# Performance work log

Hardware: AMD Instinct MI355X
Metric: run time of the kernel (lower is better)

Reference implementation:

```python
import jax, jax.numpy as jnp
import numpy as np
import math

B, C, H, W = 8, 256, 64, 64
G = 32           # norm_groups
IMG_C = 3        # image_channels * wavelet_components
EPS = 1e-5


def group_norm(x, gamma, beta):
    # x: [B, C, H, W]; normalize over (C//G, H, W) within each of G groups
    b, c, h, w = x.shape
    xg = x.reshape(b, G, c // G, h, w)
    mean = xg.mean(axis=(2, 3, 4), keepdims=True)
    var = xg.var(axis=(2, 3, 4), keepdims=True)
    xg = (xg - mean) * jax.lax.rsqrt(var + EPS)
    x = xg.reshape(b, c, h, w)
    return x * gamma[None, :, None, None] + beta[None, :, None, None]


def conv1x1(x, weight):
    # weight: [out_c, in_c]; 1x1 conv == channel matmul
    return jnp.einsum('oc,bchw->bohw', weight, x)


def setup_inputs() -> dict:
    key = jax.random.key(0)
    ks = jax.random.split(key, 8)
    s_q = 1.0 / math.sqrt(IMG_C)
    s_kv = 1.0 / math.sqrt(C)
    return {
        'input': jax.random.normal(ks[0], (B, C, H, W), jnp.float32),
        'quary': jax.random.normal(ks[1], (B, IMG_C, H, W), jnp.float32),
        'gn_weight': jnp.ones((C,), jnp.float32),
        'gn_bias': jnp.zeros((C,), jnp.float32),
        'w_q': jax.random.uniform(ks[2], (C, IMG_C), jnp.float32, -s_q, s_q),
        'w_kv': jax.random.uniform(ks[3], (2 * C, C), jnp.float32, -s_kv, s_kv),
        'w_out': jax.random.uniform(ks[4], (C, C), jnp.float32, -s_kv, s_kv),
        'b_out': jax.random.uniform(ks[5], (C,), jnp.float32, -s_kv, s_kv),
    }


def reference(input, quary, gn_weight, gn_bias, w_q, w_kv, w_out, b_out):
    b, c, h, w = input.shape
    norm = group_norm(input, gn_weight, gn_bias)
    kv = conv1x1(norm, w_kv)                      # [B, 2C, H, W]
    key_t, value = kv[:, :c], kv[:, c:]           # each [B, C, H, W]
    q = conv1x1(quary, w_q)                       # [B, C, H, W]
    # attention over all spatial positions, single head, head_dim = C
    attn = jnp.einsum('bchw,bcyx->bhwyx', q, key_t) / math.sqrt(c)
    attn = jax.nn.softmax(attn.reshape(b, h, w, h * w), axis=-1)
    attn = attn.reshape(b, h, w, h, w)
    out = jnp.einsum('bhwyx,bcyx->bchw', attn, value)  # [B, C, H, W]
    out = conv1x1(out, w_out) + b_out[None, :, None, None]
    return out + input
```

## Files before the change

### kernel.cpp

```cpp
#include <hip/hip_runtime.h>

typedef unsigned short u16;
typedef unsigned int   u32;
typedef float  f32x4  __attribute__((ext_vector_type(4)));
typedef float  fltx4  __attribute__((ext_vector_type(4)));
typedef float  f32x2  __attribute__((ext_vector_type(2)));
typedef short  bf16x8 __attribute__((ext_vector_type(8)));
typedef u32    u32x4  __attribute__((ext_vector_type(4)));
typedef u32    u32x2  __attribute__((ext_vector_type(2)));

#define CDIM 256
#define NPIX 4096
#define QSCALE 0.09016843736f

__device__ __forceinline__ u16 f2bf(float f) {
  u32 u = __builtin_bit_cast(u32, f);
  u += 0x7fffu + ((u >> 16) & 1u);
  return (u16)(u >> 16);
}
__device__ __forceinline__ float bf2f(u16 h) {
  return __builtin_bit_cast(float, (u32)h << 16);
}

#if __has_builtin(__builtin_amdgcn_exp2f)
#define FEXP2 __builtin_amdgcn_exp2f
#else
#define FEXP2 exp2f
#endif

#define LO2(v) __builtin_shufflevector(v, v, 0, 1)
#define HI2(v) __builtin_shufflevector(v, v, 2, 3)

union U8 { bf16x8 v; u16 u[8]; u32 w[4]; };

__device__ __forceinline__ void llds16(u16* lds_base, const u16* gsrc) {
  __builtin_amdgcn_global_load_lds(
      (const __attribute__((address_space(1))) unsigned int*)gsrc,
      (__attribute__((address_space(3))) unsigned int*)lds_base, 16, 0, 0);
}

__global__ __launch_bounds__(256) void prep(const float* __restrict__ wkv,
                                            const float* __restrict__ wout,
                                            const float* __restrict__ wq,
                                            u16* __restrict__ w16,
                                            float* __restrict__ wq3p) {
  const int blk = blockIdx.x, tid = threadIdx.x;
  if (blk < 4) {
    const float* s = (blk < 2 ? wkv + 65536 : wout) + (blk & 1) * 32768;
    u16* d = w16 + (blk >> 1) * 65536 + (blk & 1) * 32768;
    for (int i = tid * 4; i < 32768; i += 1024) {
      fltx4 v = *(const fltx4*)(s + i);
      u32x2 o;
      o[0] = (u32)f2bf(v[0]) | ((u32)f2bf(v[1]) << 16);
      o[1] = (u32)f2bf(v[2]) | ((u32)f2bf(v[3]) << 16);
      *(u32x2*)(d + i) = o;
    }
  } else {
    const int p = blk - 4, c = tid;
    float a0 = 0.f, a1 = 0.f, a2 = 0.f;
    for (int o = p * 64; o < p * 64 + 64; ++o) {
      float kv = wkv[o * 256 + c];
      a0 += wq[o * 3 + 0] * kv;
      a1 += wq[o * 3 + 1] * kv;
      a2 += wq[o * 3 + 2] * kv;
    }
    float* dst = wq3p + (p * 256 + c) * 4;
    dst[0] = a0 * QSCALE; dst[1] = a1 * QSCALE; dst[2] = a2 * QSCALE; dst[3] = 0.f;
  }
}

__global__ __launch_bounds__(1024) void gn_stats(const float* __restrict__ x,
                                                 float* __restrict__ stats) {
  int bg = blockIdx.x;
  const float* base = x + (long)bg * 32768;
  float s = 0.f, s2 = 0.f;
  for (int i = threadIdx.x; i < 8192; i += 1024) {
    fltx4 v = ((const fltx4*)base)[i];
    s  += v[0] + v[1] + v[2] + v[3];
    s2 += v[0]*v[0] + v[1]*v[1] + v[2]*v[2] + v[3]*v[3];
  }
  for (int off = 1; off < 64; off <<= 1) {
    s  += __shfl_xor(s, off);
    s2 += __shfl_xor(s2, off);
  }
  __shared__ float red[32];
  int w = threadIdx.x >> 6;
  if ((threadIdx.x & 63) == 0) { red[w] = s; red[16 + w] = s2; }
  __syncthreads();
  if (threadIdx.x < 16) {
    s  = red[threadIdx.x];
    s2 = red[16 + threadIdx.x];
    for (int off = 1; off < 16; off <<= 1) {
      s  += __shfl_xor(s, off);
      s2 += __shfl_xor(s2, off);
    }
    if (threadIdx.x == 0) {
      float mean = s * (1.f / 32768.f);
      float var  = s2 * (1.f / 32768.f) - mean * mean;
      stats[bg * 2]     = mean;
      stats[bg * 2 + 1] = rsqrtf(var + 1e-5f);
    }
  }
}

#define TSTR 264
__global__ __launch_bounds__(256) void gn_fused(const float* __restrict__ x,
                                                const float* __restrict__ stats,
                                                const float* __restrict__ gamma,
                                                const float* __restrict__ beta,
                                                const float* __restrict__ wq3p,
                                                const u16* __restrict__ w16v,
                                                u16* __restrict__ Vv,
                                                float* __restrict__ K3x,
                                                float* __restrict__ K3y,
                                                float* __restrict__ K3z) {
  __shared__ u16 tile[64 * TSTR];
  __shared__ float wl4[256 * 4];
  __shared__ float part[4][64][4];
  const int tid = threadIdx.x;
  const int b = blockIdx.y, nb = blockIdx.x * 64;
  const int nIn = tid & 63, c4 = tid >> 6;
  const int lane = tid & 63;
  const int m = lane & 15, quad = lane >> 4;
  {
    const f32x4* wp = (const f32x4*)wq3p;
    *(f32x4*)&wl4[tid * 4] = wp[tid] + wp[256 + tid] + wp[512 + tid] + wp[768 + tid];
  }
  const float* xb = x + (long)b * (CDIM * NPIX);
  #pragma unroll
  for (int p8 = 0; p8 < 8; ++p8) {
    U8 pk;
    #pragma unroll
    for (int e = 0; e < 8; ++e) {
      int c = c4 * 64 + p8 * 8 + e;
      int g = c >> 3;
      float mean = stats[(b * 32 + g) * 2];
      float rstd = stats[(b * 32 + g) * 2 + 1];
      float v = xb[(long)c * NPIX + nb + nIn];
      pk.u[e] = f2bf((v - mean) * rstd * gamma[c] + beta[c]);
    }
    *(bf16x8*)&tile[nIn * TSTR + c4 * 64 + p8 * 8] = pk.v;
  }
  __syncthreads();
  {
    float a0 = 0.f, a1 = 0.f, a2 = 0.f;
    #pragma unroll
    for (int p8 = 0; p8 < 8; ++p8) {
      U8 v; v.v = *(const bf16x8*)&tile[nIn * TSTR + c4 * 64 + p8 * 8];
      #pragma unroll
      for (int e = 0; e < 8; ++e) {
        int c = c4 * 64 + p8 * 8 + e;
        float f = bf2f(v.u[e]);
        const f32x4 wv = *(const f32x4*)&wl4[c * 4];
        a0 += f * wv[0]; a1 += f * wv[1]; a2 += f * wv[2];
      }
    }
    part[c4][nIn][0] = a0; part[c4][nIn][1] = a1; part[c4][nIn][2] = a2;
  }
  __syncthreads();
  if (c4 == 0) {
    float s0 = part[0][nIn][0] + part[1][nIn][0] + part[2][nIn][0] + part[3][nIn][0];
    float s1 = part[0][nIn][1] + part[1][nIn][1] + part[2][nIn][1] + part[3][nIn][1];
    float s2 = part[0][nIn][2] + part[1][nIn][2] + part[2][nIn][2] + part[3][nIn][2];
    long idx = (long)b * NPIX + nb + nIn;
    K3x[idx] = s0; K3y[idx] = s1; K3z[idx] = s2;
  }
  f32x4 acc[4][4] = {};
  #pragma unroll
  for (int ks = 0; ks < 8; ++ks) {
    const int kb = ks * 32;
    bf16x8 av[4], bv[4];
    #pragma unroll
    for (int i = 0; i < 4; ++i)
      av[i] = *(const bf16x8*)&w16v[(c4 * 64 + i * 16 + m) * 256 + kb + quad * 8];
    #pragma unroll
    for (int i = 0; i < 4; ++i)
      bv[i] = *(const bf16x8*)&tile[(i * 16 + m) * TSTR + kb + quad * 8];
    #pragma unroll
    for (int mi = 0; mi < 4; ++mi)
      #pragma unroll
      for (int ni = 0; ni < 4; ++ni)
        acc[mi][ni] = __builtin_amdgcn_mfma_f32_16x16x32_bf16(av[mi], bv[ni], acc[mi][ni], 0, 0, 0);
  }
  u16* Vb = Vv + (long)b * (CDIM * NPIX);
  #pragma unroll
  for (int mi = 0; mi < 4; ++mi)
    #pragma unroll
    for (int r = 0; r < 4; ++r) {
      int o = c4 * 64 + mi * 16 + quad * 4 + r;
      #pragma unroll
      for (int ni = 0; ni < 4; ++ni)
        Vb[(long)o * NPIX + nb + ni * 16 + m] = f2bf(acc[mi][ni][r]);
    }
}

template <bool FINAL, int WAYS>
__global__ __launch_bounds__(256, 2) void gemm_nt(
    const void* __restrict__ Ap,
    const void* __restrict__ B0, const void* __restrict__ B1,
    const float* __restrict__ ls,
    void* __restrict__ Dp,
    const float* __restrict__ bias, const float* __restrict__ resid,
    int M, int N, long aBS, long bBS, long dBS, long rBS) {
  __shared__ u16 Als[128 * 72];
  __shared__ u16 Bls[128 * 72];
  __shared__ float invB[128];
  const int tid = threadIdx.x;
  const int lane = tid & 63;
  const int m = lane & 15, quad = lane >> 4;
  const int wid = tid >> 6;
  const int wm = wid & 1, wn = wid >> 1;
  const int m0 = blockIdx.x * 128, n0 = blockIdx.y * 128;
  const int bz = blockIdx.z;

  if constexpr (WAYS > 0) {
    if (tid < 128) {
      long n = (long)bz * 4096 + n0 + tid;
      invB[tid] = 1.f / (ls[n] + ls[32768 + n]);
    }
    __syncthreads();
  }

  f32x4 acc[4][4] = {};

  for (int ks = 0; ks < 4; ++ks) {
    const int kb = ks * 64;
    if (ks) __syncthreads();
    {
      const u16* src = (const u16*)Ap + aBS * bz;
      #pragma unroll
      for (int it = 0; it < 4; ++it) {
        int idx = it * 2048 + tid * 8;
        int r = idx >> 6, c = idx & 63;
        *(u32x4*)&Als[r * 72 + c] = *(const u32x4*)(src + (long)(m0 + r) * CDIM + kb + c);
      }
    }
    if constexpr (WAYS > 0) {
      const u16* s0 = (const u16*)B0 + bBS * bz;
      const u16* s1 = (const u16*)B1 + bBS * bz;
      #pragma unroll
      for (int it = 0; it < 4; ++it) {
        int idx = it * 2048 + tid * 8;
        int r = idx >> 6, c = idx & 63;
        long off = (long)(n0 + r) * CDIM + kb + c;
        u32x4 A0 = *(const u32x4*)(s0 + off);
        u32x4 A1 = *(const u32x4*)(s1 + off);
        float inv = invB[r];
        u32x4 o;
        #pragma unroll
        for (int i = 0; i < 4; ++i) {
          float lo = (bf2f((u16)(A0[i] & 0xffff)) + bf2f((u16)(A1[i] & 0xffff))) * inv;
          float hi = (bf2f((u16)(A0[i] >> 16))    + bf2f((u16)(A1[i] >> 16)))    * inv;
          o[i] = (u32)f2bf(lo) | ((u32)f2bf(hi) << 16);
        }
        *(u32x4*)&Bls[r * 72 + c] = o;
      }
    } else {
      const u16* src = (const u16*)B0 + bBS * bz;
      #pragma unroll
      for (int it = 0; it < 4; ++it) {
        int idx = it * 2048 + tid * 8;
        int r = idx >> 6, c = idx & 63;
        *(u32x4*)&Bls[r * 72 + c] = *(const u32x4*)(src + (long)(n0 + r) * CDIM + kb + c);
      }
    }
    __syncthreads();
    #pragma unroll
    for (int s = 0; s < 2; ++s) {
      bf16x8 av[4], bv[4];
      #pragma unroll
      for (int i = 0; i < 4; ++i)
        av[i] = *(const bf16x8*)&Als[(wm * 64 + i * 16 + m) * 72 + s * 32 + quad * 8];
      #pragma unroll
      for (int i = 0; i < 4; ++i)
        bv[i] = *(const bf16x8*)&Bls[(wn * 64 + i * 16 + m) * 72 + s * 32 + quad * 8];
      #pragma unroll
      for (int mi = 0; mi < 4; ++mi)
        #pragma unroll
        for (int ni = 0; ni < 4; ++ni)
          acc[mi][ni] = __builtin_amdgcn_mfma_f32_16x16x32_bf16(av[mi], bv[ni], acc[mi][ni], 0, 0, 0);
    }
  }

  const int row0 = m0 + wm * 64;
  const int col0 = n0 + wn * 64 + m;
  if constexpr (FINAL) {
    float* out = (float*)Dp + dBS * bz;
    const float* res = resid + rBS * bz;
    #pragma unroll
    for (int mi = 0; mi < 4; ++mi)
      #pragma unroll
      for (int r = 0; r < 4; ++r) {
        int row = row0 + mi * 16 + quad * 4 + r;
        float bs = bias[row];
        #pragma unroll
        for (int ni = 0; ni < 4; ++ni) {
          long off = (long)row * N + col0 + ni * 16;
          out[off] = acc[mi][ni][r] + bs + res[off];
        }
      }
  } else {
    u16* out = (u16*)Dp + dBS * bz;
    #pragma unroll
    for (int mi = 0; mi < 4; ++mi)
      #pragma unroll
      for (int r = 0; r < 4; ++r) {
        int row = row0 + mi * 16 + quad * 4 + r;
        #pragma unroll
        for (int ni = 0; ni < 4; ++ni)
          out[(long)row * N + col0 + ni * 16] = f2bf(acc[mi][ni][r]);
      }
  }
}

#define MFMA16(a, bfr, c) __builtin_amdgcn_mfma_f32_16x16x32_bf16(a, bfr, c, 0, 0, 0)

#define P_LOAD(ks, JB)                                                      \
  {                                                                         \
    const int jo_ = (JB) + (ks) * 32 + quad * 8;                            \
    kx0 = *(const fltx4*)(Kx + jo_); kx1 = *(const fltx4*)(Kx + jo_ + 4);   \
    ky0 = *(const fltx4*)(Ky + jo_); ky1 = *(const fltx4*)(Ky + jo_ + 4);   \
    kz0 = *(const fltx4*)(Kz + jo_); kz1 = *(const fltx4*)(Kz + jo_ + 4);   \
  }

#define P_EXP(PB, ks)                                                       \
  {                                                                         \
    f32x2 xc_[4] = {LO2(kx0), HI2(kx0), LO2(kx1), HI2(kx1)};                \
    f32x2 yc_[4] = {LO2(ky0), HI2(ky0), LO2(ky1), HI2(ky1)};                \
    f32x2 zc_[4] = {LO2(kz0), HI2(kz0), LO2(kz1), HI2(kz1)};                \
    _Pragma("unroll")                                                       \
    for (int qm_ = 0; qm_ < 2; ++qm_) {                                     \
      _Pragma("unroll")                                                     \
      for (int c2_ = 0; c2_ < 4; ++c2_) {                                   \
        f32x2 s_ = xc_[c2_] * y2[qm_][0] + yc_[c2_] * y2[qm_][1]            \
                 + zc_[c2_] * y2[qm_][2];                                   \
        float p0_ = FEXP2(s_[0]);                                           \
        float p1_ = FEXP2(s_[1]);                                           \
        u32 r0_ = __builtin_bit_cast(u32, p0_) + 0x8000u;                   \
        u32 r1_ = __builtin_bit_cast(u32, p1_) + 0x8000u;                   \
        PB[qm_][ks].w[c2_] = (r0_ >> 16) | (r1_ & 0xffff0000u);             \
        f32x2 pv_; pv_[0] = p0_; pv_[1] = p1_;                              \
        lsv[qm_] += pv_;                                                    \
      }                                                                     \
    }                                                                       \
  }

#define PV_GROUP(PB, CT0)                                                   \
  _Pragma("unroll")                                                         \
  for (int ct_ = (CT0); ct_ < (CT0) + 4; ++ct_) {                           \
    int c_ = ct_ * 16 + m;                                                  \
    bf16x8 a0_ = *(const bf16x8*)&Vb[c_ * 64 + (((quad)     ^ (c_ & 7)) << 3)]; \
    bf16x8 a1_ = *(const bf16x8*)&Vb[c_ * 64 + (((4 + quad) ^ (c_ & 7)) << 3)]; \
    acc[0][ct_] = MFMA16(a0_, PB[0][0].v, acc[0][ct_]);                     \
    acc[1][ct_] = MFMA16(a0_, PB[1][0].v, acc[1][ct_]);                     \
    acc[0][ct_] = MFMA16(a1_, PB[0][1].v, acc[0][ct_]);                     \
    acc[1][ct_] = MFMA16(a1_, PB[1][1].v, acc[1][ct_]);                     \
  }

__global__ __launch_bounds__(256, 2) void attn_kernel(
    const float* __restrict__ quary,
    const float* __restrict__ K3x, const float* __restrict__ K3y,
    const float* __restrict__ K3z,
    const u16* __restrict__ V, u16* __restrict__ Op0, u16* __restrict__ Op1,
    float* __restrict__ lsum) {
  __shared__ u16 VLS[2][256 * 64];
  const int lane = threadIdx.x & 63, w = threadIdx.x >> 6;
  const int m = lane & 15, quad = lane >> 4;
  const int b = blockIdx.z, half = blockIdx.y;
  const int qb = blockIdx.x * 128 + w * 32;

  f32x2 y2[2][3];
  #pragma unroll
  for (int qm = 0; qm < 2; ++qm) {
    int n = qb + qm * 16 + m;
    float q0 = quary[b * 12288 + n];
    float q1 = quary[b * 12288 + 4096 + n];
    float q2 = quary[b * 12288 + 8192 + n];
    y2[qm][0][0] = q0; y2[qm][0][1] = q0;
    y2[qm][1][0] = q1; y2[qm][1][1] = q1;
    y2[qm][2][0] = q2; y2[qm][2][1] = q2;
  }

  const float* Kx = K3x + (long)b * NPIX + half * 2048;
  const float* Ky = K3y + (long)b * NPIX + half * 2048;
  const float* Kz = K3z + (long)b * NPIX + half * 2048;
  const u16* VG = V + (long)b * CDIM * NPIX + half * 2048;

  int srcV[8];
  #pragma unroll
  for (int i = 0; i < 8; ++i) {
    int c = (w * 8 + i) * 8 + (lane >> 3);
    srcV[i] = c * NPIX + (((lane & 7) ^ (c & 7)) << 3);
  }

  f32x2 lsv[2] = {};
  f32x4 acc[2][16] = {};
  U8 pbA[2][2], pbB[2][2];
  fltx4 kx0, kx1, ky0, ky1, kz0, kz1;

  #pragma unroll
  for (int i = 0; i < 8; ++i)
    llds16(VLS[0] + (w * 8 + i) * 512, VG + srcV[i]);

  P_LOAD(0, 0); P_EXP(pbA, 0);
  P_LOAD(1, 0); P_EXP(pbA, 1);

  for (int kt = 0; kt < 31; ++kt) {
    __syncthreads();
    #pragma unroll
    for (int i = 0; i < 8; ++i)
      llds16(VLS[(kt + 1) & 1] + (w * 8 + i) * 512, VG + srcV[i] + (kt + 1) * 64);
    const u16* Vb = VLS[kt & 1];
    const int JB = (kt + 1) * 64;

    P_LOAD(0, JB);
    PV_GROUP(pbA, 0);
    PV_GROUP(pbA, 4);
    P_EXP(pbB, 0);
    P_LOAD(1, JB);
    PV_GROUP(pbA, 8);
    PV_GROUP(pbA, 12);
    P_EXP(pbB, 1);

    pbA[0][0] = pbB[0][0]; pbA[0][1] = pbB[0][1];
    pbA[1][0] = pbB[1][0]; pbA[1][1] = pbB[1][1];
  }
  {
    __syncthreads();
    const u16* Vb = VLS[1];
    PV_GROUP(pbA, 0);
    PV_GROUP(pbA, 4);
    PV_GROUP(pbA, 8);
    PV_GROUP(pbA, 12);
  }

  u16* OpB = (half ? Op1 : Op0);
  #pragma unroll
  for (int qm = 0; qm < 2; ++qm) {
    int n = qb + qm * 16 + m;
    u16* row = OpB + ((long)b * NPIX + n) * CDIM + quad * 4;
    #pragma unroll
    for (int ct = 0; ct < 16; ++ct) {
      u32x2 o;
      o[0] = (u32)f2bf(acc[qm][ct][0]) | ((u32)f2bf(acc[qm][ct][1]) << 16);
      o[1] = (u32)f2bf(acc[qm][ct][2]) | ((u32)f2bf(acc[qm][ct][3]) << 16);
      *(u32x2*)(row + ct * 16) = o;
    }
    float ls = lsv[qm][0] + lsv[qm][1];
    ls += __shfl_xor(ls, 16);
    ls += __shfl_xor(ls, 32);
    if (lane < 16)
      lsum[(long)half * 32768 + (long)b * NPIX + n] = ls;
  }
}

extern "C" void kernel_launch(void* const* d_in, const int* in_sizes, int n_in,
                              void* d_out, int out_size, void* d_ws, size_t ws_size,
                              hipStream_t stream) {
  (void)in_sizes; (void)n_in; (void)out_size; (void)ws_size;
  const float* input = (const float*)d_in[0];
  const float* quary = (const float*)d_in[1];
  const float* gnw   = (const float*)d_in[2];
  const float* gnb   = (const float*)d_in[3];
  const float* wq    = (const float*)d_in[4];
  const float* wkv   = (const float*)d_in[5];
  const float* wout  = (const float*)d_in[6];
  const float* bout  = (const float*)d_in[7];
  float* out = (float*)d_out;

  char* ws = (char*)d_ws;
  float* stats = (float*)ws;
  float* wq3p  = (float*)(ws + 4096);
  float* lsum  = (float*)(ws + 20480);
  float* K3x   = (float*)(ws + 282624);
  float* K3y   = (float*)(ws + 413696);
  float* K3z   = (float*)(ws + 544768);
  u16* w16   = (u16*)(ws + 675840);
  const long base = 937984;
  u16* Vv    = (u16*)(ws + base);
  u16* Op0   = (u16*)(ws + base + 1L * 16777216);
  u16* Op1   = (u16*)(ws + base + 2L * 16777216);

  const long S = (long)NPIX * CDIM;

  prep<<<8, 256, 0, stream>>>(wkv, wout, wq, w16, wq3p);
  gn_stats<<<256, 1024, 0, stream>>>(input, stats);
  gn_fused<<<dim3(64, 8), 256, 0, stream>>>(input, stats, gnw, gnb, wq3p,
                                            w16, Vv, K3x, K3y, K3z);
  attn_kernel<<<dim3(32, 2, 8), 256, 0, stream>>>(quary, K3x, K3y, K3z, Vv, Op0, Op1, lsum);
  gemm_nt<true, 2><<<dim3(2, 32, 8), 256, 0, stream>>>(
      w16 + 65536, Op0, Op1, lsum, out, bout, input, 256, 4096, 0, S, S, S);
}
```

Before: 233.1 us.

## Merge prep into gn_stats, retile output GEMM, raise PV MFMA priority

Folds the weight-conversion prep kernel into the group-norm statistics kernel as extra blocks, which removes one launch. The output projection GEMM moves from 128x128 to 64x128 tiles with a higher occupancy hint, giving 1024 blocks instead of 512 for better CU fill. The attention kernel also wraps its PV MFMA groups in s_setprio so they get issue priority over the exp work. The trade-offs are that the B operand, including its dual-source combine, is now loaded and converted twice as often, and the priority hints may or may not change scheduling.

```diff
diff --git a/kernel.cpp b/kernel.cpp
--- a/kernel.cpp
+++ b/kernel.cpp
@@ -39,23 +39,55 @@
       (__attribute__((address_space(3))) unsigned int*)lds_base, 16, 0, 0);
 }
 
-__global__ __launch_bounds__(256) void prep(const float* __restrict__ wkv,
-                                            const float* __restrict__ wout,
-                                            const float* __restrict__ wq,
-                                            u16* __restrict__ w16,
-                                            float* __restrict__ wq3p) {
-  const int blk = blockIdx.x, tid = threadIdx.x;
+__global__ __launch_bounds__(1024) void gn_stats_prep(
+    const float* __restrict__ x, const float* __restrict__ wkv,
+    const float* __restrict__ wout, const float* __restrict__ wq,
+    float* __restrict__ stats, u16* __restrict__ w16, float* __restrict__ wq3p) {
+  const int bid = blockIdx.x, tid = threadIdx.x;
+  if (bid < 256) {
+    const float* base = x + (long)bid * 32768;
+    float s = 0.f, s2 = 0.f;
+    for (int i = tid; i < 8192; i += 1024) {
+      fltx4 v = ((const fltx4*)base)[i];
+      s  += v[0] + v[1] + v[2] + v[3];
+      s2 += v[0]*v[0] + v[1]*v[1] + v[2]*v[2] + v[3]*v[3];
+    }
+    for (int off = 1; off < 64; off <<= 1) {
+      s  += __shfl_xor(s, off);
+      s2 += __shfl_xor(s2, off);
+    }
+    __shared__ float red[32];
+    int w = tid >> 6;
+    if ((tid & 63) == 0) { red[w] = s; red[16 + w] = s2; }
+    __syncthreads();
+    if (tid < 16) {
+      s  = red[tid];
+      s2 = red[16 + tid];
+      for (int off = 1; off < 16; off <<= 1) {
+        s  += __shfl_xor(s, off);
+        s2 += __shfl_xor(s2, off);
+      }
+      if (tid == 0) {
+        float mean = s * (1.f / 32768.f);
+        float var  = s2 * (1.f / 32768.f) - mean * mean;
+        stats[bid * 2]     = mean;
+        stats[bid * 2 + 1] = rsqrtf(var + 1e-5f);
+      }
+    }
+    return;
+  }
+  const int blk = bid - 256;
   if (blk < 4) {
     const float* s = (blk < 2 ? wkv + 65536 : wout) + (blk & 1) * 32768;
     u16* d = w16 + (blk >> 1) * 65536 + (blk & 1) * 32768;
-    for (int i = tid * 4; i < 32768; i += 1024) {
+    for (int i = tid * 4; i < 32768; i += 4096) {
       fltx4 v = *(const fltx4*)(s + i);
       u32x2 o;
       o[0] = (u32)f2bf(v[0]) | ((u32)f2bf(v[1]) << 16);
       o[1] = (u32)f2bf(v[2]) | ((u32)f2bf(v[3]) << 16);
       *(u32x2*)(d + i) = o;
     }
-  } else {
+  } else if (tid < 256) {
     const int p = blk - 4, c = tid;
     float a0 = 0.f, a1 = 0.f, a2 = 0.f;
     for (int o = p * 64; o < p * 64 + 64; ++o) {
@@ -66,40 +98,6 @@
     }
     float* dst = wq3p + (p * 256 + c) * 4;
     dst[0] = a0 * QSCALE; dst[1] = a1 * QSCALE; dst[2] = a2 * QSCALE; dst[3] = 0.f;
-  }
-}
-
-__global__ __launch_bounds__(1024) void gn_stats(const float* __restrict__ x,
-                                                 float* __restrict__ stats) {
-  int bg = blockIdx.x;
-  const float* base = x + (long)bg * 32768;
-  float s = 0.f, s2 = 0.f;
-  for (int i = threadIdx.x; i < 8192; i += 1024) {
-    fltx4 v = ((const fltx4*)base)[i];
-    s  += v[0] + v[1] + v[2] + v[3];
-    s2 += v[0]*v[0] + v[1]*v[1] + v[2]*v[2] + v[3]*v[3];
-  }
-  for (int off = 1; off < 64; off <<= 1) {
-    s  += __shfl_xor(s, off);
-    s2 += __shfl_xor(s2, off);
-  }
-  __shared__ float red[32];
-  int w = threadIdx.x >> 6;
-  if ((threadIdx.x & 63) == 0) { red[w] = s; red[16 + w] = s2; }
-  __syncthreads();
-  if (threadIdx.x < 16) {
-    s  = red[threadIdx.x];
-    s2 = red[16 + threadIdx.x];
-    for (int off = 1; off < 16; off <<= 1) {
-      s  += __shfl_xor(s, off);
-      s2 += __shfl_xor(s2, off);
-    }
-    if (threadIdx.x == 0) {
-      float mean = s * (1.f / 32768.f);
-      float var  = s2 * (1.f / 32768.f) - mean * mean;
-      stats[bg * 2]     = mean;
-      stats[bg * 2 + 1] = rsqrtf(var + 1e-5f);
-    }
   }
 }
 
@@ -194,15 +192,12 @@
     }
 }
 
-template <bool FINAL, int WAYS>
-__global__ __launch_bounds__(256, 2) void gemm_nt(
-    const void* __restrict__ Ap,
-    const void* __restrict__ B0, const void* __restrict__ B1,
-    const float* __restrict__ ls,
-    void* __restrict__ Dp,
-    const float* __restrict__ bias, const float* __restrict__ resid,
-    int M, int N, long aBS, long bBS, long dBS, long rBS) {
-  __shared__ u16 Als[128 * 72];
+__global__ __launch_bounds__(256, 4) void gemm_out(
+    const u16* __restrict__ Ap, const u16* __restrict__ B0,
+    const u16* __restrict__ B1, const float* __restrict__ ls,
+    float* __restrict__ out, const float* __restrict__ bias,
+    const float* __restrict__ resid) {
+  __shared__ u16 Als[64 * 72];
   __shared__ u16 Bls[128 * 72];
   __shared__ float invB[128];
   const int tid = threadIdx.x;
@@ -210,34 +205,30 @@
   const int m = lane & 15, quad = lane >> 4;
   const int wid = tid >> 6;
   const int wm = wid & 1, wn = wid >> 1;
-  const int m0 = blockIdx.x * 128, n0 = blockIdx.y * 128;
+  const int m0 = blockIdx.x * 64, n0 = blockIdx.y * 128;
   const int bz = blockIdx.z;
-
-  if constexpr (WAYS > 0) {
-    if (tid < 128) {
-      long n = (long)bz * 4096 + n0 + tid;
-      invB[tid] = 1.f / (ls[n] + ls[32768 + n]);
-    }
-    __syncthreads();
-  }
-
-  f32x4 acc[4][4] = {};
+  const long S = (long)NPIX * CDIM;
+
+  if (tid < 128) {
+    long n = (long)bz * 4096 + n0 + tid;
+    invB[tid] = 1.f / (ls[n] + ls[32768 + n]);
+  }
+  __syncthreads();
+
+  f32x4 acc[2][4] = {};
 
   for (int ks = 0; ks < 4; ++ks) {
     const int kb = ks * 64;
     if (ks) __syncthreads();
+    #pragma unroll
+    for (int it = 0; it < 2; ++it) {
+      int idx = it * 2048 + tid * 8;
+      int r = idx >> 6, c = idx & 63;
+      *(u32x4*)&Als[r * 72 + c] = *(const u32x4*)(Ap + (long)(m0 + r) * CDIM + kb + c);
+    }
     {
-      const u16* src = (const u16*)Ap + aBS * bz;
-      #pragma unroll
-      for (int it = 0; it < 4; ++it) {
-        int idx = it * 2048 + tid * 8;
-        int r = idx >> 6, c = idx & 63;
-        *(u32x4*)&Als[r * 72 + c] = *(const u32x4*)(src + (long)(m0 + r) * CDIM + kb + c);
-      }
-    }
-    if constexpr (WAYS > 0) {
-      const u16* s0 = (const u16*)B0 + bBS * bz;
-      const u16* s1 = (const u16*)B1 + bBS * bz;
+      const u16* s0 = B0 + S * bz;
+      const u16* s1 = B1 + S * bz;
       #pragma unroll
       for (int it = 0; it < 4; ++it) {
         int idx = it * 2048 + tid * 8;
@@ -255,62 +246,41 @@
         }
         *(u32x4*)&Bls[r * 72 + c] = o;
       }
-    } else {
-      const u16* src = (const u16*)B0 + bBS * bz;
-      #pragma unroll
-      for (int it = 0; it < 4; ++it) {
-        int idx = it * 2048 + tid * 8;
-        int r = idx >> 6, c = idx & 63;
-        *(u32x4*)&Bls[r * 72 + c] = *(const u32x4*)(src + (long)(n0 + r) * CDIM + kb + c);
-      }
     }
     __syncthreads();
     #pragma unroll
     for (int s = 0; s < 2; ++s) {
-      bf16x8 av[4], bv[4];
-      #pragma unroll
-      for (int i = 0; i < 4; ++i)
-        av[i] = *(const bf16x8*)&Als[(wm * 64 + i * 16 + m) * 72 + s * 32 + quad * 8];
+      bf16x8 av[2], bv[4];
+      #pragma unroll
+      for (int i = 0; i < 2; ++i)
+        av[i] = *(const bf16x8*)&Als[(wm * 32 + i * 16 + m) * 72 + s * 32 + quad * 8];
       #pragma unroll
       for (int i = 0; i < 4; ++i)
         bv[i] = *(const bf16x8*)&Bls[(wn * 64 + i * 16 + m) * 72 + s * 32 + quad * 8];
       #pragma unroll
-      for (int mi = 0; mi < 4; ++mi)
+      for (int mi = 0; mi < 2; ++mi)
         #pragma unroll
         for (int ni = 0; ni < 4; ++ni)
           acc[mi][ni] = __builtin_amdgcn_mfma_f32_16x16x32_bf16(av[mi], bv[ni], acc[mi][ni], 0, 0, 0);
     }
   }
 
-  const int row0 = m0 + wm * 64;
+  const int row0 = m0 + wm * 32;
   const int col0 = n0 + wn * 64 + m;
-  if constexpr (FINAL) {
-    float* out = (float*)Dp + dBS * bz;
-    const float* res = resid + rBS * bz;
-    #pragma unroll
-    for (int mi = 0; mi < 4; ++mi)
-      #pragma unroll
-      for (int r = 0; r < 4; ++r) {
-        int row = row0 + mi * 16 + quad * 4 + r;
-        float bs = bias[row];
-        #pragma unroll
-        for (int ni = 0; ni < 4; ++ni) {
-          long off = (long)row * N + col0 + ni * 16;
-          out[off] = acc[mi][ni][r] + bs + res[off];
-        }
+  float* ob = out + S * bz;
+  const float* res = resid + S * bz;
+  #pragma unroll
+  for (int mi = 0; mi < 2; ++mi)
+    #pragma unroll
+    for (int r = 0; r < 4; ++r) {
+      int row = row0 + mi * 16 + quad * 4 + r;
+      float bs = bias[row];
+      #pragma unroll
+      for (int ni = 0; ni < 4; ++ni) {
+        long off = (long)row * NPIX + col0 + ni * 16;
+        ob[off] = acc[mi][ni][r] + bs + res[off];
       }
-  } else {
-    u16* out = (u16*)Dp + dBS * bz;
-    #pragma unroll
-    for (int mi = 0; mi < 4; ++mi)
-      #pragma unroll
-      for (int r = 0; r < 4; ++r) {
-        int row = row0 + mi * 16 + quad * 4 + r;
-        #pragma unroll
-        for (int ni = 0; ni < 4; ++ni)
-          out[(long)row * N + col0 + ni * 16] = f2bf(acc[mi][ni][r]);
-      }
-  }
+    }
 }
 
 #define MFMA16(a, bfr, c) __builtin_amdgcn_mfma_f32_16x16x32_bf16(a, bfr, c, 0, 0, 0)
@@ -414,12 +384,16 @@
     const int JB = (kt + 1) * 64;
 
     P_LOAD(0, JB);
+    __builtin_amdgcn_s_setprio(1);
     PV_GROUP(pbA, 0);
     PV_GROUP(pbA, 4);
+    __builtin_amdgcn_s_setprio(0);
     P_EXP(pbB, 0);
     P_LOAD(1, JB);
+    __builtin_amdgcn_s_setprio(1);
     PV_GROUP(pbA, 8);
     PV_GROUP(pbA, 12);
+    __builtin_amdgcn_s_setprio(0);
     P_EXP(pbB, 1);
 
     pbA[0][0] = pbB[0][0]; pbA[0][1] = pbB[0][1];
@@ -428,10 +402,12 @@
   {
     __syncthreads();
     const u16* Vb = VLS[1];
+    __builtin_amdgcn_s_setprio(1);
     PV_GROUP(pbA, 0);
     PV_GROUP(pbA, 4);
     PV_GROUP(pbA, 8);
     PV_GROUP(pbA, 12);
+    __builtin_amdgcn_s_setprio(0);
   }
 
   u16* OpB = (half ? Op1 : Op0);
@@ -481,13 +457,10 @@
   u16* Op0   = (u16*)(ws + base + 1L * 16777216);
   u16* Op1   = (u16*)(ws + base + 2L * 16777216);
 
-  const long S = (long)NPIX * CDIM;
-
-  prep<<<8, 256, 0, stream>>>(wkv, wout, wq, w16, wq3p);
-  gn_stats<<<256, 1024, 0, stream>>>(input, stats);
+  gn_stats_prep<<<264, 1024, 0, stream>>>(input, wkv, wout, wq, stats, w16, wq3p);
   gn_fused<<<dim3(64, 8), 256, 0, stream>>>(input, stats, gnw, gnb, wq3p,
                                             w16, Vv, K3x, K3y, K3z);
   attn_kernel<<<dim3(32, 2, 8), 256, 0, stream>>>(quary, K3x, K3y, K3z, Vv, Op0, Op1, lsum);
-  gemm_nt<true, 2><<<dim3(2, 32, 8), 256, 0, stream>>>(
-      w16 + 65536, Op0, Op1, lsum, out, bout, input, 256, 4096, 0, S, S, S);
-}
+  gemm_out<<<dim3(4, 32, 8), 256, 0, stream>>>(
+      w16 + 65536, Op0, Op1, lsum, out, bout, input);
+}
```

After: 235.9 us. No clear change (+1.2%).
